# Kernel tuning notes

Hardware: AMD Instinct MI355X
Metric: run time of the kernel (lower is better)

Reference implementation:

```python
import jax, jax.numpy as jnp
import numpy as np

IN_CAPS, OUT_CAPS, OUT_DIM = 32, 10, 16


def squash(s):
    # s: [B, out_caps, out_dim]
    sq = jnp.sum(s * s, axis=2)              # [B, out_caps]
    mod = jnp.sqrt(sq)
    scale = sq / (1.0 + sq) / mod            # matches torch: sqrmod/(1+sqrmod)/mod
    return scale[..., None] * s


def setup_inputs() -> dict:
    key = jax.random.key(0)
    k1, k2 = jax.random.split(key)
    B, in_dim = 4096, 288
    caps_output = jax.random.normal(k1, (B, IN_CAPS, in_dim), dtype=jnp.float32)
    # W initialized uniform(-1/32, 1/32) in the original; scale randn similarly small
    W = jax.random.uniform(k2, (IN_CAPS, in_dim, OUT_CAPS * OUT_DIM),
                           dtype=jnp.float32, minval=-1.0 / 32, maxval=1.0 / 32)
    b = jnp.zeros((IN_CAPS, OUT_CAPS), dtype=jnp.float32)
    return {"caps_output": caps_output, "W": W, "b": b}


def reference(caps_output, W, b):
    B = caps_output.shape[0]
    # caps_output.unsqueeze(2).matmul(W): per-input-capsule matmul
    u = jnp.einsum('bni,nio->bno', caps_output, W)          # [B, 32, 160]
    u = u.reshape(B, IN_CAPS, OUT_CAPS, OUT_DIM)            # [B, 32, 10, 16]

    c = jax.nn.softmax(b, axis=1)                           # [32, 10]
    s = jnp.einsum('no,bnod->bod', c, u)                    # [B, 10, 16]
    v = squash(s)

    b_batch = jnp.broadcast_to(b, (B, IN_CAPS, OUT_CAPS))
    for _ in range(3):
        # agreement: <u_predict, v>
        b_batch = b_batch + jnp.einsum('bnod,bod->bno', u, v)
        c = jax.nn.softmax(b_batch, axis=-1)                # [B, 32, 10]
        s = jnp.einsum('bno,bnod->bod', c, u)
        v = squash(s)
    return v
```

## Files before the change

kernel.cpp:

```cpp
#include <hip/hip_runtime.h>
#include <hip/hip_bf16.h>

#define IN_CAPS 32
#define OUT_CAPS 10
#define NOUT 160
#define KDIM 288
#define BATCH 4096
#define KSTEPS 9
#define CTILES 10
#define STR2 162

typedef __bf16 bf16x8 __attribute__((ext_vector_type(8)));
typedef float  f32x4  __attribute__((ext_vector_type(4)));

__global__ __launch_bounds__(256) void prep_w(const float* __restrict__ W,
                                              __bf16* __restrict__ Wf) {
    int f = blockIdx.x * 256 + threadIdx.x;
    int j    = f & 7;
    int l    = (f >> 3) & 63;
    int rest = f >> 9;
    int c    = rest % CTILES;
    int tnk  = rest / CTILES;
    int ks   = tnk % KSTEPS;
    int n    = tnk / KSTEPS;
    int k    = ks * 32 + (l >> 4) * 8 + j;
    int col  = c * 16 + (l & 15);
    Wf[f] = (__bf16)W[(n * KDIM + k) * NOUT + col];
}

__global__ __launch_bounds__(256) void gemm_u(const float* __restrict__ caps,
                                              const __bf16* __restrict__ Wf,
                                              uint4* __restrict__ up) {
    const int n    = blockIdx.y;
    const int wave = threadIdx.x >> 6;
    const int lane = threadIdx.x & 63;
    const int rw   = blockIdx.x * 4 + wave;
    const int lm   = lane & 15;
    const int lk   = lane >> 4;

    f32x4 acc[2][CTILES];
#pragma unroll
    for (int mt = 0; mt < 2; ++mt)
#pragma unroll
        for (int ct = 0; ct < CTILES; ++ct)
            acc[mt][ct] = (f32x4){0.f, 0.f, 0.f, 0.f};

    const float* a0 = caps + (size_t)(rw * 32 + lm) * (IN_CAPS * KDIM) + n * KDIM + lk * 8;
    const float* a1 = a0 + (size_t)16 * (IN_CAPS * KDIM);
    const __bf16* wfn = Wf + (size_t)n * (KSTEPS * CTILES * 512) + lane * 8;

    f32x4 pre[4];
    pre[0] = *(const f32x4*)(a0);
    pre[1] = *(const f32x4*)(a0 + 4);
    pre[2] = *(const f32x4*)(a1);
    pre[3] = *(const f32x4*)(a1 + 4);

    for (int ks = 0; ks < KSTEPS; ++ks) {
        bf16x8 afr[2];
#pragma unroll
        for (int mt = 0; mt < 2; ++mt) {
            bf16x8 a;
            a[0] = (__bf16)pre[2*mt][0]; a[1] = (__bf16)pre[2*mt][1];
            a[2] = (__bf16)pre[2*mt][2]; a[3] = (__bf16)pre[2*mt][3];
            a[4] = (__bf16)pre[2*mt+1][0]; a[5] = (__bf16)pre[2*mt+1][1];
            a[6] = (__bf16)pre[2*mt+1][2]; a[7] = (__bf16)pre[2*mt+1][3];
            afr[mt] = a;
        }
        if (ks + 1 < KSTEPS) {
            const float* n0 = a0 + (ks + 1) * 32;
            const float* n1 = a1 + (ks + 1) * 32;
            pre[0] = *(const f32x4*)(n0);
            pre[1] = *(const f32x4*)(n0 + 4);
            pre[2] = *(const f32x4*)(n1);
            pre[3] = *(const f32x4*)(n1 + 4);
        }
        const __bf16* wks = wfn + (size_t)ks * (CTILES * 512);
#pragma unroll
        for (int ct = 0; ct < CTILES; ++ct) {
            bf16x8 bfr = *(const bf16x8*)(wks + ct * 512);
            acc[0][ct] = __builtin_amdgcn_mfma_f32_16x16x32_bf16(afr[0], bfr, acc[0][ct], 0, 0, 0);
            acc[1][ct] = __builtin_amdgcn_mfma_f32_16x16x32_bf16(afr[1], bfr, acc[1][ct], 0, 0, 0);
        }
    }

    const size_t cbase = (((size_t)n * 128 + rw) * 2) * 5 * 64 + lane;
#pragma unroll
    for (int mt = 0; mt < 2; ++mt)
#pragma unroll
        for (int p = 0; p < 5; ++p) {
            bf16x8 pk;
#pragma unroll
            for (int j = 0; j < 8; ++j)
                pk[j] = (__bf16)acc[mt][2 * p + (j >> 2)][j & 3];
            up[cbase + ((size_t)mt * 5 + p) * 64] = __builtin_bit_cast(uint4, pk);
        }
}

__global__ __launch_bounds__(256) void routing(const uint4* __restrict__ up,
                                               const float* __restrict__ bbias,
                                               float* __restrict__ out) {
    __shared__ __bf16 ul[4][IN_CAPS * STR2];
    __shared__ float  bl[4][IN_CAPS * OUT_CAPS];
    __shared__ float  cs[4][IN_CAPS * OUT_CAPS];
    __shared__ float  ss[4][NOUT];
    __shared__ float  vs[4][NOUT];
    __shared__ float  scale_s[4][16];

    const int t  = threadIdx.x;
    const int b0 = blockIdx.x * 4;
    const int rw = b0 >> 5;
    const int mt = (b0 >> 4) & 1;
    const int lk = (b0 >> 2) & 3;

    for (int c = t; c < 2560; c += 256) {
        int n   = c / 80;
        int rem = c - n * 80;
        int p   = rem >> 4;
        int lm  = rem & 15;
        size_t idx = ((((size_t)n * 128 + rw) * 2 + mt) * 5 + p) * 64 + lk * 16 + lm;
        bf16x8 v = __builtin_bit_cast(bf16x8, up[idx]);
#pragma unroll
        for (int j = 0; j < 8; ++j) {
            int ct = 2 * p + (j >> 2);
            int rr = j & 3;
            ul[rr][n * STR2 + ct * 16 + lm] = v[j];
        }
    }
    const int grp = t >> 6;
    const int g   = t & 63;
    for (int pp = g; pp < IN_CAPS * OUT_CAPS; pp += 64) bl[grp][pp] = bbias[pp];
    __syncthreads();

    for (int it = 0; it < 4; ++it) {
        if (it > 0) {
            for (int pp = g; pp < IN_CAPS * OUT_CAPS; pp += 64) {
                int n = pp & 31;
                int o = pp >> 5;
                float a = 0.f;
#pragma unroll
                for (int d = 0; d < 16; ++d)
                    a += (float)ul[grp][n * STR2 + o * 16 + d] * vs[grp][o * 16 + d];
                bl[grp][n * 10 + o] += a;
            }
            __syncthreads();
        }
        if (g < IN_CAPS) {
            float m = bl[grp][g * 10];
#pragma unroll
            for (int o = 1; o < 10; ++o) m = fmaxf(m, bl[grp][g * 10 + o]);
            float e[10];
            float sum = 0.f;
#pragma unroll
            for (int o = 0; o < 10; ++o) { e[o] = __expf(bl[grp][g * 10 + o] - m); sum += e[o]; }
            float inv = 1.0f / sum;
#pragma unroll
            for (int o = 0; o < 10; ++o) cs[grp][g * 10 + o] = e[o] * inv;
        }
        __syncthreads();
        for (int p = g; p < NOUT; p += 64) {
            int o = p >> 4;
            float a = 0.f;
#pragma unroll
            for (int n = 0; n < IN_CAPS; ++n)
                a += cs[grp][n * 10 + o] * (float)ul[grp][n * STR2 + p];
            ss[grp][p] = a;
        }
        __syncthreads();
        if (g < OUT_CAPS) {
            float sq = 0.f;
#pragma unroll
            for (int d = 0; d < 16; ++d) { float x = ss[grp][g * 16 + d]; sq += x * x; }
            scale_s[grp][g] = sq / ((1.0f + sq) * sqrtf(sq));
        }
        __syncthreads();
        for (int p = g; p < NOUT; p += 64) vs[grp][p] = scale_s[grp][p >> 4] * ss[grp][p];
        __syncthreads();
    }

    for (int p = g; p < NOUT; p += 64)
        out[(size_t)(b0 + grp) * NOUT + p] = vs[grp][p];
}

extern "C" void kernel_launch(void* const* d_in, const int* in_sizes, int n_in,
                              void* d_out, int out_size, void* d_ws, size_t ws_size,
                              hipStream_t stream) {
    const float* caps  = (const float*)d_in[0];
    const float* W     = (const float*)d_in[1];
    const float* bbias = (const float*)d_in[2];
    float* out = (float*)d_out;

    __bf16* Wf = (__bf16*)d_ws;
    uint4*  up = (uint4*)((char*)d_ws + 2949120);

    prep_w<<<dim3(5760), dim3(256), 0, stream>>>(W, Wf);
    gemm_u<<<dim3(32, 32), dim3(256), 0, stream>>>(caps, Wf, up);
    routing<<<dim3(BATCH / 4), dim3(256), 0, stream>>>(up, bbias, out);
}
```

Measured before the change: 82.22 us.

## Stream caps tiles into LDS via async global_load_lds with triple buffering

The GEMM kernel now stages activation tiles through a swizzled, triple-buffered LDS ring filled by async global-to-LDS loads, paced with explicit vmcnt waits. This replaces register prefetch and aims to keep more loads in flight while the MFMAs run. Each wave now computes one 16-row tile instead of two, and the grid is doubled to raise parallelism and cut register pressure. In exchange, each block reuses every W fragment across half as many rows, which increases W fragment traffic, and the scheme relies on hand-written waitcnt ordering.

```diff
diff --git a/kernel.cpp b/kernel.cpp
--- a/kernel.cpp
+++ b/kernel.cpp
@@ -12,6 +12,8 @@
 
 typedef __bf16 bf16x8 __attribute__((ext_vector_type(8)));
 typedef float  f32x4  __attribute__((ext_vector_type(4)));
+typedef __attribute__((address_space(1))) void as1_t;
+typedef __attribute__((address_space(3))) void as3_t;
 
 __global__ __launch_bounds__(256) void prep_w(const float* __restrict__ W,
                                               __bf16* __restrict__ Wf) {
@@ -31,69 +33,79 @@
 __global__ __launch_bounds__(256) void gemm_u(const float* __restrict__ caps,
                                               const __bf16* __restrict__ Wf,
                                               uint4* __restrict__ up) {
+    __shared__ float abuf[3][64 * 32];
+
     const int n    = blockIdx.y;
-    const int wave = threadIdx.x >> 6;
+    const int rb   = blockIdx.x;
+    const int w    = threadIdx.x >> 6;
     const int lane = threadIdx.x & 63;
-    const int rw   = blockIdx.x * 4 + wave;
     const int lm   = lane & 15;
     const int lk   = lane >> 4;
 
-    f32x4 acc[2][CTILES];
-#pragma unroll
-    for (int mt = 0; mt < 2; ++mt)
-#pragma unroll
-        for (int ct = 0; ct < CTILES; ++ct)
-            acc[mt][ct] = (f32x4){0.f, 0.f, 0.f, 0.f};
-
-    const float* a0 = caps + (size_t)(rw * 32 + lm) * (IN_CAPS * KDIM) + n * KDIM + lk * 8;
-    const float* a1 = a0 + (size_t)16 * (IN_CAPS * KDIM);
+    const int s0 = w * 128 + lane;
+    const int s1 = s0 + 64;
+    const int r0 = s0 >> 3;
+    const int r1 = s1 >> 3;
+    const int c0 = (s0 & 7) ^ (r0 & 7);
+    const int c1 = (s1 & 7) ^ (r1 & 7);
+    const float* g0 = caps + (size_t)(rb * 64 + r0) * (IN_CAPS * KDIM) + n * KDIM + c0 * 4;
+    const float* g1 = caps + (size_t)(rb * 64 + r1) * (IN_CAPS * KDIM) + n * KDIM + c1 * 4;
+
+    f32x4 acc[CTILES];
+#pragma unroll
+    for (int ct = 0; ct < CTILES; ++ct) acc[ct] = (f32x4){0.f, 0.f, 0.f, 0.f};
+
+    const int rloc = w * 16 + lm;
+    const int h0   = ((lk * 2)     ^ (lm & 7)) * 4;
+    const int h1   = ((lk * 2 + 1) ^ (lm & 7)) * 4;
     const __bf16* wfn = Wf + (size_t)n * (KSTEPS * CTILES * 512) + lane * 8;
 
-    f32x4 pre[4];
-    pre[0] = *(const f32x4*)(a0);
-    pre[1] = *(const f32x4*)(a0 + 4);
-    pre[2] = *(const f32x4*)(a1);
-    pre[3] = *(const f32x4*)(a1 + 4);
-
+    __builtin_amdgcn_global_load_lds((const as1_t*)g0, (as3_t*)&abuf[0][w * 512],       16, 0, 0);
+    __builtin_amdgcn_global_load_lds((const as1_t*)g1, (as3_t*)&abuf[0][w * 512 + 256], 16, 0, 0);
+    __builtin_amdgcn_global_load_lds((const as1_t*)(g0 + 32), (as3_t*)&abuf[1][w * 512],       16, 0, 0);
+    __builtin_amdgcn_global_load_lds((const as1_t*)(g1 + 32), (as3_t*)&abuf[1][w * 512 + 256], 16, 0, 0);
+
+#pragma unroll
     for (int ks = 0; ks < KSTEPS; ++ks) {
-        bf16x8 afr[2];
-#pragma unroll
-        for (int mt = 0; mt < 2; ++mt) {
-            bf16x8 a;
-            a[0] = (__bf16)pre[2*mt][0]; a[1] = (__bf16)pre[2*mt][1];
-            a[2] = (__bf16)pre[2*mt][2]; a[3] = (__bf16)pre[2*mt][3];
-            a[4] = (__bf16)pre[2*mt+1][0]; a[5] = (__bf16)pre[2*mt+1][1];
-            a[6] = (__bf16)pre[2*mt+1][2]; a[7] = (__bf16)pre[2*mt+1][3];
-            afr[mt] = a;
-        }
-        if (ks + 1 < KSTEPS) {
-            const float* n0 = a0 + (ks + 1) * 32;
-            const float* n1 = a1 + (ks + 1) * 32;
-            pre[0] = *(const f32x4*)(n0);
-            pre[1] = *(const f32x4*)(n0 + 4);
-            pre[2] = *(const f32x4*)(n1);
-            pre[3] = *(const f32x4*)(n1 + 4);
-        }
+        if (ks + 1 < KSTEPS) asm volatile("s_waitcnt vmcnt(2)" ::: "memory");
+        else                 asm volatile("s_waitcnt vmcnt(0)" ::: "memory");
+
+        const float* bc = abuf[ks % 3];
+        f32x4 x0 = *(const f32x4*)&bc[rloc * 32 + h0];
+        f32x4 x1 = *(const f32x4*)&bc[rloc * 32 + h1];
+        bf16x8 a;
+        a[0] = (__bf16)x0[0]; a[1] = (__bf16)x0[1];
+        a[2] = (__bf16)x0[2]; a[3] = (__bf16)x0[3];
+        a[4] = (__bf16)x1[0]; a[5] = (__bf16)x1[1];
+        a[6] = (__bf16)x1[2]; a[7] = (__bf16)x1[3];
+
         const __bf16* wks = wfn + (size_t)ks * (CTILES * 512);
 #pragma unroll
         for (int ct = 0; ct < CTILES; ++ct) {
             bf16x8 bfr = *(const bf16x8*)(wks + ct * 512);
-            acc[0][ct] = __builtin_amdgcn_mfma_f32_16x16x32_bf16(afr[0], bfr, acc[0][ct], 0, 0, 0);
-            acc[1][ct] = __builtin_amdgcn_mfma_f32_16x16x32_bf16(afr[1], bfr, acc[1][ct], 0, 0, 0);
-        }
-    }
-
-    const size_t cbase = (((size_t)n * 128 + rw) * 2) * 5 * 64 + lane;
-#pragma unroll
-    for (int mt = 0; mt < 2; ++mt)
-#pragma unroll
-        for (int p = 0; p < 5; ++p) {
-            bf16x8 pk;
-#pragma unroll
-            for (int j = 0; j < 8; ++j)
-                pk[j] = (__bf16)acc[mt][2 * p + (j >> 2)][j & 3];
-            up[cbase + ((size_t)mt * 5 + p) * 64] = __builtin_bit_cast(uint4, pk);
-        }
+            acc[ct] = __builtin_amdgcn_mfma_f32_16x16x32_bf16(a, bfr, acc[ct], 0, 0, 0);
+        }
+
+        if (ks + 2 < KSTEPS) {
+            float* dst = &abuf[(ks + 2) % 3][0];
+            __builtin_amdgcn_global_load_lds((const as1_t*)(g0 + (ks + 2) * 32),
+                                             (as3_t*)(dst + w * 512),       16, 0, 0);
+            __builtin_amdgcn_global_load_lds((const as1_t*)(g1 + (ks + 2) * 32),
+                                             (as3_t*)(dst + w * 512 + 256), 16, 0, 0);
+        }
+    }
+
+    const int rw = rb * 2 + (w >> 1);
+    const int mt = w & 1;
+    const size_t cbase = ((((size_t)n * 128 + rw) * 2 + mt) * 5) * 64 + lane;
+#pragma unroll
+    for (int p = 0; p < 5; ++p) {
+        bf16x8 pk;
+#pragma unroll
+        for (int j = 0; j < 8; ++j)
+            pk[j] = (__bf16)acc[2 * p + (j >> 2)][j & 3];
+        up[cbase + (size_t)p * 64] = __builtin_bit_cast(uint4, pk);
+    }
 }
 
 __global__ __launch_bounds__(256) void routing(const uint4* __restrict__ up,
@@ -161,8 +173,8 @@
             int o = p >> 4;
             float a = 0.f;
 #pragma unroll
-            for (int n = 0; n < IN_CAPS; ++n)
-                a += cs[grp][n * 10 + o] * (float)ul[grp][n * STR2 + p];
+            for (int nn = 0; nn < IN_CAPS; ++nn)
+                a += cs[grp][nn * 10 + o] * (float)ul[grp][nn * STR2 + p];
             ss[grp][p] = a;
         }
         __syncthreads();
@@ -193,6 +205,6 @@
     uint4*  up = (uint4*)((char*)d_ws + 2949120);
 
     prep_w<<<dim3(5760), dim3(256), 0, stream>>>(W, Wf);
-    gemm_u<<<dim3(32, 32), dim3(256), 0, stream>>>(caps, Wf, up);
+    gemm_u<<<dim3(64, 32), dim3(256), 0, stream>>>(caps, Wf, up);
     routing<<<dim3(BATCH / 4), dim3(256), 0, stream>>>(up, bbias, out);
 }
```

Result: slower. 86.61 us (+5.3%).

## Stage per-capsule W tile in LDS and deepen A prefetch in gemm_u

Applied to the files above, without the earlier changes.

gemm_u now uses 512-thread blocks covering 256 batch rows for one input capsule, and the block copies that capsule's full bf16 W slice (about 92 KB) into shared memory once. All eight waves then read B fragments from LDS instead of each wave loading them from global/L2. The activation prefetch is also deepened from one to three K-steps in registers, with the K loop fully unrolled. The large LDS footprint limits occupancy to about one block per CU, and the extra prefetch registers add register pressure.

```diff
diff --git a/kernel.cpp b/kernel.cpp
--- a/kernel.cpp
+++ b/kernel.cpp
@@ -28,16 +28,41 @@
     Wf[f] = (__bf16)W[(n * KDIM + k) * NOUT + col];
 }
 
-__global__ __launch_bounds__(256) void gemm_u(const float* __restrict__ caps,
+__global__ __launch_bounds__(512) void gemm_u(const float* __restrict__ caps,
                                               const __bf16* __restrict__ Wf,
                                               uint4* __restrict__ up) {
-    const int n    = blockIdx.y;
-    const int wave = threadIdx.x >> 6;
+    __shared__ __bf16 Bs[KSTEPS * 5120];
+
+    const int lin  = blockIdx.x;
+    const int n    = lin & 31;
+    const int rg   = lin >> 5;
+    const int w    = threadIdx.x >> 6;
     const int lane = threadIdx.x & 63;
-    const int rw   = blockIdx.x * 4 + wave;
     const int lm   = lane & 15;
     const int lk   = lane >> 4;
 
+    {
+        const uint4* wsrc = (const uint4*)(Wf + (size_t)n * (KSTEPS * 5120));
+        uint4* bdst = (uint4*)Bs;
+#pragma unroll
+        for (int i = 0; i < 11; ++i)
+            bdst[threadIdx.x + i * 512] = wsrc[threadIdx.x + i * 512];
+        if (threadIdx.x < 128) bdst[threadIdx.x + 11 * 512] = wsrc[threadIdx.x + 11 * 512];
+    }
+
+    const int row0 = rg * 256 + w * 32;
+    const float* a0 = caps + ((size_t)(row0 + lm) * IN_CAPS + n) * KDIM + lk * 8;
+    const float* a1 = a0 + (size_t)16 * IN_CAPS * KDIM;
+
+    f32x4 pre[3][4];
+#pragma unroll
+    for (int s = 0; s < 3; ++s) {
+        pre[s][0] = *(const f32x4*)(a0 + s * 32);
+        pre[s][1] = *(const f32x4*)(a0 + s * 32 + 4);
+        pre[s][2] = *(const f32x4*)(a1 + s * 32);
+        pre[s][3] = *(const f32x4*)(a1 + s * 32 + 4);
+    }
+
     f32x4 acc[2][CTILES];
 #pragma unroll
     for (int mt = 0; mt < 2; ++mt)
@@ -45,55 +70,50 @@
         for (int ct = 0; ct < CTILES; ++ct)
             acc[mt][ct] = (f32x4){0.f, 0.f, 0.f, 0.f};
 
-    const float* a0 = caps + (size_t)(rw * 32 + lm) * (IN_CAPS * KDIM) + n * KDIM + lk * 8;
-    const float* a1 = a0 + (size_t)16 * (IN_CAPS * KDIM);
-    const __bf16* wfn = Wf + (size_t)n * (KSTEPS * CTILES * 512) + lane * 8;
-
-    f32x4 pre[4];
-    pre[0] = *(const f32x4*)(a0);
-    pre[1] = *(const f32x4*)(a0 + 4);
-    pre[2] = *(const f32x4*)(a1);
-    pre[3] = *(const f32x4*)(a1 + 4);
-
+    __syncthreads();
+
+#pragma unroll
     for (int ks = 0; ks < KSTEPS; ++ks) {
         bf16x8 afr[2];
 #pragma unroll
         for (int mt = 0; mt < 2; ++mt) {
+            f32x4 x0 = pre[ks % 3][2 * mt];
+            f32x4 x1 = pre[ks % 3][2 * mt + 1];
             bf16x8 a;
-            a[0] = (__bf16)pre[2*mt][0]; a[1] = (__bf16)pre[2*mt][1];
-            a[2] = (__bf16)pre[2*mt][2]; a[3] = (__bf16)pre[2*mt][3];
-            a[4] = (__bf16)pre[2*mt+1][0]; a[5] = (__bf16)pre[2*mt+1][1];
-            a[6] = (__bf16)pre[2*mt+1][2]; a[7] = (__bf16)pre[2*mt+1][3];
+            a[0] = (__bf16)x0[0]; a[1] = (__bf16)x0[1];
+            a[2] = (__bf16)x0[2]; a[3] = (__bf16)x0[3];
+            a[4] = (__bf16)x1[0]; a[5] = (__bf16)x1[1];
+            a[6] = (__bf16)x1[2]; a[7] = (__bf16)x1[3];
             afr[mt] = a;
         }
-        if (ks + 1 < KSTEPS) {
-            const float* n0 = a0 + (ks + 1) * 32;
-            const float* n1 = a1 + (ks + 1) * 32;
-            pre[0] = *(const f32x4*)(n0);
-            pre[1] = *(const f32x4*)(n0 + 4);
-            pre[2] = *(const f32x4*)(n1);
-            pre[3] = *(const f32x4*)(n1 + 4);
-        }
-        const __bf16* wks = wfn + (size_t)ks * (CTILES * 512);
+        if (ks + 3 < KSTEPS) {
+            pre[ks % 3][0] = *(const f32x4*)(a0 + (ks + 3) * 32);
+            pre[ks % 3][1] = *(const f32x4*)(a0 + (ks + 3) * 32 + 4);
+            pre[ks % 3][2] = *(const f32x4*)(a1 + (ks + 3) * 32);
+            pre[ks % 3][3] = *(const f32x4*)(a1 + (ks + 3) * 32 + 4);
+        }
+        const __bf16* Bc = &Bs[ks * 5120 + lane * 8];
 #pragma unroll
         for (int ct = 0; ct < CTILES; ++ct) {
-            bf16x8 bfr = *(const bf16x8*)(wks + ct * 512);
+            bf16x8 bfr = *(const bf16x8*)(Bc + ct * 512);
             acc[0][ct] = __builtin_amdgcn_mfma_f32_16x16x32_bf16(afr[0], bfr, acc[0][ct], 0, 0, 0);
             acc[1][ct] = __builtin_amdgcn_mfma_f32_16x16x32_bf16(afr[1], bfr, acc[1][ct], 0, 0, 0);
         }
     }
 
-    const size_t cbase = (((size_t)n * 128 + rw) * 2) * 5 * 64 + lane;
-#pragma unroll
-    for (int mt = 0; mt < 2; ++mt)
+    const int rw = (rg * 256 + w * 32) >> 5;
+#pragma unroll
+    for (int mt = 0; mt < 2; ++mt) {
+        const size_t cbase = ((((size_t)n * 128 + rw) * 2 + mt) * 5) * 64 + lane;
 #pragma unroll
         for (int p = 0; p < 5; ++p) {
             bf16x8 pk;
 #pragma unroll
             for (int j = 0; j < 8; ++j)
                 pk[j] = (__bf16)acc[mt][2 * p + (j >> 2)][j & 3];
-            up[cbase + ((size_t)mt * 5 + p) * 64] = __builtin_bit_cast(uint4, pk);
-        }
+            up[cbase + (size_t)p * 64] = __builtin_bit_cast(uint4, pk);
+        }
+    }
 }
 
 __global__ __launch_bounds__(256) void routing(const uint4* __restrict__ up,
@@ -161,8 +181,8 @@
             int o = p >> 4;
             float a = 0.f;
 #pragma unroll
-            for (int n = 0; n < IN_CAPS; ++n)
-                a += cs[grp][n * 10 + o] * (float)ul[grp][n * STR2 + p];
+            for (int nn = 0; nn < IN_CAPS; ++nn)
+                a += cs[grp][nn * 10 + o] * (float)ul[grp][nn * STR2 + p];
             ss[grp][p] = a;
         }
         __syncthreads();
@@ -193,6 +213,6 @@
     uint4*  up = (uint4*)((char*)d_ws + 2949120);
 
     prep_w<<<dim3(5760), dim3(256), 0, stream>>>(W, Wf);
-    gemm_u<<<dim3(32, 32), dim3(256), 0, stream>>>(caps, Wf, up);
+    gemm_u<<<dim3(512), dim3(512), 0, stream>>>(caps, Wf, up);
     routing<<<dim3(BATCH / 4), dim3(256), 0, stream>>>(up, bbias, out);
 }
```

Measured after the change: 78.63 us. 4.4% less time.
